# Performance work log

Measured on AMD Instinct MI355X. Metric: run time of the kernel, lower is better.

## Reference

```python
import jax, jax.numpy as jnp
import numpy as np


def l2norm(t, eps=1e-12):
    # matches F.normalize(p=2, dim=-1): divide by norm clamped to eps
    n = jnp.linalg.norm(t, axis=-1, keepdims=True)
    return t / jnp.maximum(n, eps)


def setup_inputs() -> dict:
    key = jax.random.key(0)
    kx, ke = jax.random.split(key)
    B, N, D, C = 8, 1024, 256, 8192
    x = jax.random.normal(kx, (B, N, D), dtype=jnp.float32)
    # codebook initialized l2-normalized, as in __init__ (kmeans_init=False)
    embed = l2norm(jax.random.normal(ke, (1, C, D), dtype=jnp.float32))
    return {"x": x, "embed": embed}


def reference(x, embed):
    # x: [B, N, D]; ndim < 4 -> add codebook dim h=1
    xh = x[None]                                   # [1, B, N, D]
    h, b, n, d = xh.shape
    flat = l2norm(xh.reshape(h, b * n, d))         # [1, B*N, D]
    e = l2norm(embed)                              # [1, C, D]
    # cosine-similarity distances
    dist = jnp.einsum('hnd,hcd->hnc', flat, e)     # [1, B*N, C]
    # sample_codebook_temp == 0 -> plain argmax
    idx = jnp.argmax(dist, axis=-1).reshape(h, b, n)  # [1, B, N]
    # batched_embedding: gather UN-normalized codebook rows
    quantize = jax.vmap(lambda em, ix: em[ix])(embed, idx)  # [1, B, N, D]
    # needs_codebook_dim -> strip leading dim
    return quantize[0], idx[0]
```

## Files before the change

kernel.cpp:

```cpp
#include <hip/hip_runtime.h>
#include <math.h>

#define QROWS 8192
#define DDIM  256
#define CCNT  8192
#define BM    128
#define BN    128
#define BK    64
#define CBLKS (CCNT / BN)

typedef __attribute__((ext_vector_type(4))) float f32x4;
typedef __attribute__((ext_vector_type(8))) short bf16x8;

__device__ __forceinline__ unsigned short f2bf(float f) {
    unsigned u = __float_as_uint(f);
    u += 0x7fffu + ((u >> 16) & 1u);
    return (unsigned short)(u >> 16);
}
__device__ __forceinline__ unsigned u32max(unsigned a, unsigned b) { return a > b ? a : b; }
__device__ __forceinline__ unsigned u32min(unsigned a, unsigned b) { return a < b ? a : b; }

__device__ __forceinline__ unsigned key32(float v, unsigned enc) {
    unsigned u = __float_as_uint(v);
    unsigned s = (unsigned)((int)u >> 31);
    return ((u ^ (s | 0x80000000u)) & 0xFFFFFF80u) | enc;
}

__global__ void k_prep(const float* __restrict__ x, unsigned short* __restrict__ xb,
                       const float* __restrict__ e, unsigned short* __restrict__ eb) {
    const int bid = blockIdx.x;
    if (bid < 1024) {
        const int i = (bid * 256 + threadIdx.x) * 8;
        const float4 f0 = *reinterpret_cast<const float4*>(x + i);
        const float4 f1 = *reinterpret_cast<const float4*>(x + i + 4);
        uint4 o;
        o.x = f2bf(f0.x) | ((unsigned)f2bf(f0.y) << 16);
        o.y = f2bf(f0.z) | ((unsigned)f2bf(f0.w) << 16);
        o.z = f2bf(f1.x) | ((unsigned)f2bf(f1.y) << 16);
        o.w = f2bf(f1.z) | ((unsigned)f2bf(f1.w) << 16);
        *reinterpret_cast<uint4*>(xb + i) = o;
    } else {
        const int row  = (bid - 1024) * 4 + (threadIdx.x >> 6);
        const int lane = threadIdx.x & 63;
        const float4 v = *reinterpret_cast<const float4*>(e + (size_t)row * DDIM + lane * 4);
        float s = v.x * v.x + v.y * v.y + v.z * v.z + v.w * v.w;
        #pragma unroll
        for (int off = 1; off < 64; off <<= 1) s += __shfl_xor(s, off);
        const float inv = 1.0f / fmaxf(sqrtf(s), 1e-12f);
        ushort4 o;
        o.x = f2bf(v.x * inv); o.y = f2bf(v.y * inv);
        o.z = f2bf(v.z * inv); o.w = f2bf(v.w * inv);
        *reinterpret_cast<ushort4*>(eb + (size_t)row * DDIM + lane * 4) = o;
    }
}

#define GLOAD_LDS(g, s) \
    __builtin_amdgcn_global_load_lds((const __attribute__((address_space(1))) void*)(g), \
                                     (__attribute__((address_space(3))) void*)(s), 16, 0, 0)

#define SBAR do { asm volatile("" ::: "memory"); __builtin_amdgcn_s_barrier(); \
                  asm volatile("" ::: "memory"); } while (0)
#define WAIT_LGKM0 do { asm volatile("s_waitcnt lgkmcnt(0)" ::: "memory"); \
                        __builtin_amdgcn_sched_barrier(0); } while (0)
#define WAIT_VM8 do { asm volatile("s_waitcnt vmcnt(8)" ::: "memory"); \
                      __builtin_amdgcn_sched_barrier(0); } while (0)
#define WAIT_VM0 do { asm volatile("s_waitcnt vmcnt(0)" ::: "memory"); \
                      __builtin_amdgcn_sched_barrier(0); } while (0)

__launch_bounds__(256)
__global__ void k_gemm(const unsigned short* __restrict__ xb,
                       const unsigned short* __restrict__ eb,
                       unsigned* pout ) {
    __shared__ __align__(16) char smem[65536];

    const int tid = threadIdx.x;
    const int w = tid >> 6, l = tid & 63;
    const int wr = w >> 1, wc = w & 1;
    const int lg = l >> 4, lr = l & 15;
    const int bx = blockIdx.x, by = blockIdx.y;
    const int n0 = by * BM, c0 = bx * BN;

    const f32x4 zero = {0.f, 0.f, 0.f, 0.f};
    f32x4 acc[4][4];
    #pragma unroll
    for (int i = 0; i < 4; ++i)
        #pragma unroll
        for (int j = 0; j < 4; ++j) acc[i][j] = zero;

    const int srow = tid >> 3;
    const int swzp = (tid & 7) ^ (srow & 7);
    const char* gA = (const char*)xb + (size_t)(n0 + srow) * 512 + swzp * 16;
    const char* gB = (const char*)eb + (size_t)(c0 + srow) * 512 + swzp * 16;
    const int wb = w * 1024;

#define STAGE(Ab, Bb, kb) do {                                          \
    GLOAD_LDS(gA + (kb),         smem + (Ab) + 0 * 4096 + wb);          \
    GLOAD_LDS(gA + (kb) + 16384, smem + (Ab) + 1 * 4096 + wb);          \
    GLOAD_LDS(gA + (kb) + 32768, smem + (Ab) + 2 * 4096 + wb);          \
    GLOAD_LDS(gA + (kb) + 49152, smem + (Ab) + 3 * 4096 + wb);          \
    GLOAD_LDS(gB + (kb),         smem + (Bb) + 0 * 4096 + wb);          \
    GLOAD_LDS(gB + (kb) + 16384, smem + (Bb) + 1 * 4096 + wb);          \
    GLOAD_LDS(gB + (kb) + 32768, smem + (Bb) + 2 * 4096 + wb);          \
    GLOAD_LDS(gB + (kb) + 49152, smem + (Bb) + 3 * 4096 + wb);          \
} while (0)

    const int aoff = (wr * 64 + lr) * 128;
    const int boff = (wc * 64 + lr) * 128;
    const int k0 = ((0 + lg) ^ (lr & 7)) * 16;
    const int k1 = ((4 + lg) ^ (lr & 7)) * 16;

    bf16x8 a[4][2], b[4][2];
#define READS(Ab, Bb) do {                                                           \
    _Pragma("unroll") for (int mi = 0; mi < 4; ++mi) {                               \
        a[mi][0] = *reinterpret_cast<const bf16x8*>(smem + (Ab) + aoff + mi * 2048 + k0); \
        a[mi][1] = *reinterpret_cast<const bf16x8*>(smem + (Ab) + aoff + mi * 2048 + k1); \
    }                                                                                \
    _Pragma("unroll") for (int nj = 0; nj < 4; ++nj) {                               \
        b[nj][0] = *reinterpret_cast<const bf16x8*>(smem + (Bb) + boff + nj * 2048 + k0); \
        b[nj][1] = *reinterpret_cast<const bf16x8*>(smem + (Bb) + boff + nj * 2048 + k1); \
    }                                                                                \
} while (0)

#define MMAS() do {                                                     \
    __builtin_amdgcn_s_setprio(1);                                      \
    _Pragma("unroll") for (int kk = 0; kk < 2; ++kk)                    \
      _Pragma("unroll") for (int mi = 0; mi < 4; ++mi)                  \
        _Pragma("unroll") for (int nj = 0; nj < 4; ++nj)                \
          acc[mi][nj] = __builtin_amdgcn_mfma_f32_16x16x32_bf16(a[mi][kk], b[nj][kk], acc[mi][nj], 0, 0, 0); \
    __builtin_amdgcn_s_setprio(0);                                      \
} while (0)

    STAGE(0, 32768, 0);
    STAGE(16384, 49152, 128);
    WAIT_VM8; SBAR;

    READS(0, 32768);
    WAIT_LGKM0; SBAR;
    STAGE(0, 32768, 256);
    MMAS();
    WAIT_VM8; SBAR;
    READS(16384, 49152);
    WAIT_LGKM0; SBAR;
    STAGE(16384, 49152, 384);
    MMAS();
    WAIT_VM8; SBAR;
    READS(0, 32768);
    WAIT_LGKM0; SBAR;
    MMAS();
    WAIT_VM0; SBAR;
    READS(16384, 49152);
    WAIT_LGKM0;
    MMAS();
    __syncthreads();

    uint2* T = (uint2*)smem;
    const unsigned encbase = (unsigned)(127 - wc * 64 - lr);
    #pragma unroll
    for (int mi = 0; mi < 4; ++mi) {
        #pragma unroll
        for (int r = 0; r < 4; ++r) {
            unsigned q0 = key32(acc[mi][0][r], encbase);
            unsigned q1 = key32(acc[mi][1][r], encbase - 16);
            unsigned q2 = key32(acc[mi][2][r], encbase - 32);
            unsigned q3 = key32(acc[mi][3][r], encbase - 48);
            const unsigned m01 = u32max(q0, q1), n01 = u32min(q0, q1);
            const unsigned m23 = u32max(q2, q3), n23 = u32min(q2, q3);
            const unsigned t1 = u32max(m01, m23);
            const unsigned t2 = u32max(u32min(m01, m23), u32max(n01, n23));
            const int rloc = wr * 64 + mi * 16 + lg * 4 + r;
            uint2 p; p.x = t1; p.y = t2;
            T[rloc * 33 + wc * 16 + lr] = p;
        }
    }
    __syncthreads();

    if (tid < BM) {
        const uint2* rp = T + tid * 33;
        unsigned T1 = 0, T2 = 0;
        #pragma unroll
        for (int i = 0; i < 32; ++i) {
            const uint2 p = rp[i];
            const unsigned n1 = u32max(T1, p.x);
            const unsigned lo = u32min(T1, p.x);
            T2 = u32max(T2, u32max(lo, p.y));
            T1 = n1;
        }
        uint2 o; o.x = T1; o.y = T2;
        *reinterpret_cast<uint2*>(pout + (size_t)(n0 + tid) * 256 + bx * 2) = o;
    }
#undef STAGE
#undef READS
#undef MMAS
}

__device__ __forceinline__ unsigned long long expand_key(unsigned k, int blk) {
    const int col = blk * 128 + 127 - (int)(k & 127u);
    return ((unsigned long long)(k & 0xFFFFFF80u) << 32) | (unsigned)(~col);
}

__global__ void k_fixup(const unsigned* pk,
                        const float* __restrict__ x, const float* __restrict__ e,
                        float* out) {
    const int row = blockIdx.x * 4 + (threadIdx.x >> 6);
    const int t   = threadIdx.x & 63;
    const uint2 kv = reinterpret_cast<const uint2*>(pk + (size_t)row * 256)[t];
    unsigned long long kk0 = expand_key(kv.x, t);
    unsigned long long kk1 = expand_key(kv.y, t);

    int cand[4];
    #pragma unroll
    for (int p = 0; p < 4; ++p) {
        unsigned long long m = kk0 > kk1 ? kk0 : kk1;
        #pragma unroll
        for (int off = 1; off < 64; off <<= 1) {
            const unsigned long long o = __shfl_xor(m, off);
            if (o > m) m = o;
        }
        cand[p] = (int)(~(unsigned)m) & (CCNT - 1);
        if (kk0 == m) kk0 = 0ull;
        if (kk1 == m) kk1 = 0ull;
    }

    const float4 xv = *reinterpret_cast<const float4*>(x + (size_t)row * DDIM + t * 4);
    float best = -INFINITY; int bc = 0x7fffffff;
    #pragma unroll
    for (int p = 0; p < 4; ++p) {
        const int c = cand[p];
        const float4 ev = *reinterpret_cast<const float4*>(e + (size_t)c * DDIM + t * 4);
        float d  = xv.x * ev.x + xv.y * ev.y + xv.z * ev.z + xv.w * ev.w;
        float ss = ev.x * ev.x + ev.y * ev.y + ev.z * ev.z + ev.w * ev.w;
        #pragma unroll
        for (int off = 1; off < 64; off <<= 1) {
            d  += __shfl_xor(d, off);
            ss += __shfl_xor(ss, off);
        }
        const float v = d * (1.0f / fmaxf(sqrtf(ss), 1e-12f));
        if (v > best || (v == best && c < bc)) { best = v; bc = c; }
    }

    if (t == 0) out[(size_t)QROWS * DDIM + row] = (float)bc;
    const float4 q = *reinterpret_cast<const float4*>(e + (size_t)bc * DDIM + t * 4);
    *reinterpret_cast<float4*>(out + (size_t)row * DDIM + t * 4) = q;
}

extern "C" void kernel_launch(void* const* d_in, const int* in_sizes, int n_in,
                              void* d_out, int out_size, void* d_ws, size_t ws_size,
                              hipStream_t stream) {
    const float* x = (const float*)d_in[0];
    const float* e = (const float*)d_in[1];
    float* out = (float*)d_out;
    char* ws = (char*)d_ws;

    unsigned short* xb = (unsigned short*)ws;
    unsigned short* eb = (unsigned short*)(ws + (size_t)4 * 1024 * 1024);

    k_prep<<<3072, 256, 0, stream>>>(x, xb, e, eb);
    dim3 g2(CBLKS, QROWS / BM);
    k_gemm<<<g2, 256, 0, stream>>>(xb, eb, (unsigned*)d_out);
    k_fixup<<<QROWS / 4, 256, 0, stream>>>((const unsigned*)d_out, x, e, out);
}
```

Baseline: 65.54 us.

## Enlarge GEMM tile to 256x256 with 8 waves and looped K pipeline

```diff
diff --git a/kernel.cpp b/kernel.cpp
--- a/kernel.cpp
+++ b/kernel.cpp
@@ -4,9 +4,9 @@
 #define QROWS 8192
 #define DDIM  256
 #define CCNT  8192
-#define BM    128
-#define BN    128
-#define BK    64
+#define BM    256
+#define BN    256
+#define BK    32
 #define CBLKS (CCNT / BN)
 
 typedef __attribute__((ext_vector_type(4))) float f32x4;
@@ -23,7 +23,7 @@
 __device__ __forceinline__ unsigned key32(float v, unsigned enc) {
     unsigned u = __float_as_uint(v);
     unsigned s = (unsigned)((int)u >> 31);
-    return ((u ^ (s | 0x80000000u)) & 0xFFFFFF80u) | enc;
+    return ((u ^ (s | 0x80000000u)) & 0xFFFFFF00u) | enc;
 }
 
 __global__ void k_prep(const float* __restrict__ x, unsigned short* __restrict__ xb,
@@ -62,12 +62,12 @@
                   asm volatile("" ::: "memory"); } while (0)
 #define WAIT_LGKM0 do { asm volatile("s_waitcnt lgkmcnt(0)" ::: "memory"); \
                         __builtin_amdgcn_sched_barrier(0); } while (0)
-#define WAIT_VM8 do { asm volatile("s_waitcnt vmcnt(8)" ::: "memory"); \
+#define WAIT_VM4 do { asm volatile("s_waitcnt vmcnt(4)" ::: "memory"); \
                       __builtin_amdgcn_sched_barrier(0); } while (0)
 #define WAIT_VM0 do { asm volatile("s_waitcnt vmcnt(0)" ::: "memory"); \
                       __builtin_amdgcn_sched_barrier(0); } while (0)
 
-__launch_bounds__(256)
+__launch_bounds__(512, 2)
 __global__ void k_gemm(const unsigned short* __restrict__ xb,
                        const unsigned short* __restrict__ eb,
                        unsigned* pout ) {
@@ -75,127 +75,126 @@
 
     const int tid = threadIdx.x;
     const int w = tid >> 6, l = tid & 63;
-    const int wr = w >> 1, wc = w & 1;
+    const int wr = w >> 2, wc = w & 3;
     const int lg = l >> 4, lr = l & 15;
     const int bx = blockIdx.x, by = blockIdx.y;
     const int n0 = by * BM, c0 = bx * BN;
 
     const f32x4 zero = {0.f, 0.f, 0.f, 0.f};
-    f32x4 acc[4][4];
-    #pragma unroll
-    for (int i = 0; i < 4; ++i)
+    f32x4 acc[8][4];
+    #pragma unroll
+    for (int i = 0; i < 8; ++i)
         #pragma unroll
         for (int j = 0; j < 4; ++j) acc[i][j] = zero;
 
-    const int srow = tid >> 3;
-    const int swzp = (tid & 7) ^ (srow & 7);
-    const char* gA = (const char*)xb + (size_t)(n0 + srow) * 512 + swzp * 16;
-    const char* gB = (const char*)eb + (size_t)(c0 + srow) * 512 + swzp * 16;
+    const int srow = tid >> 2;
+    const int schk = (tid & 3) ^ ((tid >> 3) & 3);
+    const char* gA = (const char*)xb + (size_t)(n0 + srow) * 512 + schk * 16;
+    const char* gB = (const char*)eb + (size_t)(c0 + srow) * 512 + schk * 16;
     const int wb = w * 1024;
 
-#define STAGE(Ab, Bb, kb) do {                                          \
-    GLOAD_LDS(gA + (kb),         smem + (Ab) + 0 * 4096 + wb);          \
-    GLOAD_LDS(gA + (kb) + 16384, smem + (Ab) + 1 * 4096 + wb);          \
-    GLOAD_LDS(gA + (kb) + 32768, smem + (Ab) + 2 * 4096 + wb);          \
-    GLOAD_LDS(gA + (kb) + 49152, smem + (Ab) + 3 * 4096 + wb);          \
-    GLOAD_LDS(gB + (kb),         smem + (Bb) + 0 * 4096 + wb);          \
-    GLOAD_LDS(gB + (kb) + 16384, smem + (Bb) + 1 * 4096 + wb);          \
-    GLOAD_LDS(gB + (kb) + 32768, smem + (Bb) + 2 * 4096 + wb);          \
-    GLOAD_LDS(gB + (kb) + 49152, smem + (Bb) + 3 * 4096 + wb);          \
+#define STAGE(slot, t) do {                                                  \
+    GLOAD_LDS(gA + (t) * 64,         smem + (slot) * 32768 + wb);            \
+    GLOAD_LDS(gA + (t) * 64 + 65536, smem + (slot) * 32768 + 8192 + wb);     \
+    GLOAD_LDS(gB + (t) * 64,         smem + (slot) * 32768 + 16384 + wb);    \
+    GLOAD_LDS(gB + (t) * 64 + 65536, smem + (slot) * 32768 + 24576 + wb);    \
 } while (0)
 
-    const int aoff = (wr * 64 + lr) * 128;
-    const int boff = (wc * 64 + lr) * 128;
-    const int k0 = ((0 + lg) ^ (lr & 7)) * 16;
-    const int k1 = ((4 + lg) ^ (lr & 7)) * 16;
-
-    bf16x8 a[4][2], b[4][2];
-#define READS(Ab, Bb) do {                                                           \
-    _Pragma("unroll") for (int mi = 0; mi < 4; ++mi) {                               \
-        a[mi][0] = *reinterpret_cast<const bf16x8*>(smem + (Ab) + aoff + mi * 2048 + k0); \
-        a[mi][1] = *reinterpret_cast<const bf16x8*>(smem + (Ab) + aoff + mi * 2048 + k1); \
-    }                                                                                \
-    _Pragma("unroll") for (int nj = 0; nj < 4; ++nj) {                               \
-        b[nj][0] = *reinterpret_cast<const bf16x8*>(smem + (Bb) + boff + nj * 2048 + k0); \
-        b[nj][1] = *reinterpret_cast<const bf16x8*>(smem + (Bb) + boff + nj * 2048 + k1); \
-    }                                                                                \
+    const int chkx = (lr >> 1) & 3;
+    const int aoff = (wr * 128 + lr) * 64 + ((lg ^ chkx) * 16);
+    const int boff = 16384 + (wc * 64 + lr) * 64 + ((lg ^ chkx) * 16);
+
+    bf16x8 a[8], b[4];
+#define READS(slot) do {                                                                  \
+    const char* base_ = smem + (slot) * 32768;                                            \
+    _Pragma("unroll") for (int mi = 0; mi < 8; ++mi)                                      \
+        a[mi] = *reinterpret_cast<const bf16x8*>(base_ + aoff + mi * 1024);               \
+    _Pragma("unroll") for (int nj = 0; nj < 4; ++nj)                                      \
+        b[nj] = *reinterpret_cast<const bf16x8*>(base_ + boff + nj * 1024);               \
 } while (0)
 
-#define MMAS() do {                                                     \
-    __builtin_amdgcn_s_setprio(1);                                      \
-    _Pragma("unroll") for (int kk = 0; kk < 2; ++kk)                    \
-      _Pragma("unroll") for (int mi = 0; mi < 4; ++mi)                  \
-        _Pragma("unroll") for (int nj = 0; nj < 4; ++nj)                \
-          acc[mi][nj] = __builtin_amdgcn_mfma_f32_16x16x32_bf16(a[mi][kk], b[nj][kk], acc[mi][nj], 0, 0, 0); \
-    __builtin_amdgcn_s_setprio(0);                                      \
+#define MMAS() do {                                                          \
+    __builtin_amdgcn_s_setprio(1);                                           \
+    _Pragma("unroll") for (int mi = 0; mi < 8; ++mi)                         \
+      _Pragma("unroll") for (int nj = 0; nj < 4; ++nj)                       \
+        acc[mi][nj] = __builtin_amdgcn_mfma_f32_16x16x32_bf16(a[mi], b[nj], acc[mi][nj], 0, 0, 0); \
+    __builtin_amdgcn_s_setprio(0);                                           \
 } while (0)
 
-    STAGE(0, 32768, 0);
-    STAGE(16384, 49152, 128);
-    WAIT_VM8; SBAR;
-
-    READS(0, 32768);
-    WAIT_LGKM0; SBAR;
-    STAGE(0, 32768, 256);
-    MMAS();
-    WAIT_VM8; SBAR;
-    READS(16384, 49152);
-    WAIT_LGKM0; SBAR;
-    STAGE(16384, 49152, 384);
-    MMAS();
-    WAIT_VM8; SBAR;
-    READS(0, 32768);
-    WAIT_LGKM0; SBAR;
-    MMAS();
-    WAIT_VM0; SBAR;
-    READS(16384, 49152);
-    WAIT_LGKM0;
-    MMAS();
+    STAGE(0, 0);
+    STAGE(1, 1);
+    WAIT_VM4; SBAR;
+
+    #pragma unroll
+    for (int t = 0; t < 8; ++t) {
+        const int slot = t & 1;
+        READS(slot);
+        WAIT_LGKM0;
+        SBAR;
+        if (t + 2 < 8) STAGE(slot, t + 2);
+        MMAS();
+        if (t < 7) {
+            if (t < 6) { WAIT_VM4; } else { WAIT_VM0; }
+            SBAR;
+        }
+    }
     __syncthreads();
 
     uint2* T = (uint2*)smem;
-    const unsigned encbase = (unsigned)(127 - wc * 64 - lr);
-    #pragma unroll
-    for (int mi = 0; mi < 4; ++mi) {
-        #pragma unroll
-        for (int r = 0; r < 4; ++r) {
-            unsigned q0 = key32(acc[mi][0][r], encbase);
-            unsigned q1 = key32(acc[mi][1][r], encbase - 16);
-            unsigned q2 = key32(acc[mi][2][r], encbase - 32);
-            unsigned q3 = key32(acc[mi][3][r], encbase - 48);
-            const unsigned m01 = u32max(q0, q1), n01 = u32min(q0, q1);
-            const unsigned m23 = u32max(q2, q3), n23 = u32min(q2, q3);
-            const unsigned t1 = u32max(m01, m23);
-            const unsigned t2 = u32max(u32min(m01, m23), u32max(n01, n23));
-            const int rloc = wr * 64 + mi * 16 + lg * 4 + r;
-            uint2 p; p.x = t1; p.y = t2;
-            T[rloc * 33 + wc * 16 + lr] = p;
-        }
-    }
-    __syncthreads();
-
-    if (tid < BM) {
-        const uint2* rp = T + tid * 33;
-        unsigned T1 = 0, T2 = 0;
-        #pragma unroll
-        for (int i = 0; i < 32; ++i) {
-            const uint2 p = rp[i];
-            const unsigned n1 = u32max(T1, p.x);
-            const unsigned lo = u32min(T1, p.x);
-            T2 = u32max(T2, u32max(lo, p.y));
-            T1 = n1;
-        }
-        uint2 o; o.x = T1; o.y = T2;
-        *reinterpret_cast<uint2*>(pout + (size_t)(n0 + tid) * 256 + bx * 2) = o;
+    const int slotW = wc * 16 + lr;
+    const unsigned encb = 255u - (unsigned)(wc * 64 + lr);
+    #pragma unroll
+    for (int half = 0; half < 2; ++half) {
+        #pragma unroll
+        for (int m = 0; m < 4; ++m) {
+            const int mi = half * 4 + m;
+            #pragma unroll
+            for (int r = 0; r < 4; ++r) {
+                unsigned q0 = key32(acc[mi][0][r], encb);
+                unsigned q1 = key32(acc[mi][1][r], encb - 16);
+                unsigned q2 = key32(acc[mi][2][r], encb - 32);
+                unsigned q3 = key32(acc[mi][3][r], encb - 48);
+                const unsigned m01 = u32max(q0, q1), n01 = u32min(q0, q1);
+                const unsigned m23 = u32max(q2, q3), n23 = u32min(q2, q3);
+                const unsigned t1 = u32max(m01, m23);
+                const unsigned t2 = u32max(u32min(m01, m23), u32max(n01, n23));
+                const int cr = wr * 64 + m * 16 + lg * 4 + r;
+                uint2 p; p.x = t1; p.y = t2;
+                T[cr * 64 + (slotW ^ (cr & 15))] = p;
+            }
+        }
+        __syncthreads();
+        {
+            const int cr = tid >> 2, q = tid & 3;
+            unsigned T1 = 0, T2 = 0;
+            #pragma unroll
+            for (int i = 0; i < 16; ++i) {
+                const uint2 p = T[cr * 64 + ((q * 16 + i) ^ (cr & 15))];
+                const unsigned n1 = u32max(T1, p.x);
+                const unsigned lo = u32min(T1, p.x);
+                T2 = u32max(T2, u32max(lo, p.y));
+                T1 = n1;
+            }
+            #pragma unroll
+            for (int off = 1; off < 4; off <<= 1) {
+                const unsigned o1 = __shfl_xor(T1, off);
+                const unsigned o2 = __shfl_xor(T2, off);
+                const unsigned n1 = u32max(T1, o1);
+                const unsigned lo = u32min(T1, o1);
+                T2 = u32max(u32max(T2, o2), lo);
+                T1 = n1;
+            }
+            if (q == 0) {
+                const int row = n0 + (cr >> 6) * 128 + half * 64 + (cr & 63);
+                uint2 o; o.x = T1; o.y = T2;
+                *reinterpret_cast<uint2*>(pout + (size_t)row * 256 + bx * 2) = o;
+            }
+        }
+        if (half == 0) __syncthreads();
     }
 #undef STAGE
 #undef READS
 #undef MMAS
-}
-
-__device__ __forceinline__ unsigned long long expand_key(unsigned k, int blk) {
-    const int col = blk * 128 + 127 - (int)(k & 127u);
-    return ((unsigned long long)(k & 0xFFFFFF80u) << 32) | (unsigned)(~col);
 }
 
 __global__ void k_fixup(const unsigned* pk,
@@ -203,22 +202,21 @@
                         float* out) {
     const int row = blockIdx.x * 4 + (threadIdx.x >> 6);
     const int t   = threadIdx.x & 63;
-    const uint2 kv = reinterpret_cast<const uint2*>(pk + (size_t)row * 256)[t];
-    unsigned long long kk0 = expand_key(kv.x, t);
-    unsigned long long kk1 = expand_key(kv.y, t);
+    const unsigned k = pk[(size_t)row * 256 + t];
+    const int col0 = (t >> 1) * 256 + 255 - (int)(k & 255u);
+    unsigned long long kk = ((unsigned long long)(k & 0xFFFFFF00u) << 32) | (unsigned)(~col0);
 
     int cand[4];
     #pragma unroll
     for (int p = 0; p < 4; ++p) {
-        unsigned long long m = kk0 > kk1 ? kk0 : kk1;
+        unsigned long long m = kk;
         #pragma unroll
         for (int off = 1; off < 64; off <<= 1) {
             const unsigned long long o = __shfl_xor(m, off);
             if (o > m) m = o;
         }
         cand[p] = (int)(~(unsigned)m) & (CCNT - 1);
-        if (kk0 == m) kk0 = 0ull;
-        if (kk1 == m) kk1 = 0ull;
+        if (kk == m) kk = 0ull;
     }
 
     const float4 xv = *reinterpret_cast<const float4*>(x + (size_t)row * DDIM + t * 4);
@@ -256,6 +254,6 @@
 
     k_prep<<<3072, 256, 0, stream>>>(x, xb, e, eb);
     dim3 g2(CBLKS, QROWS / BM);
-    k_gemm<<<g2, 256, 0, stream>>>(xb, eb, (unsigned*)d_out);
+    k_gemm<<<g2, 512, 0, stream>>>(xb, eb, (unsigned*)d_out);
     k_fixup<<<QROWS / 4, 256, 0, stream>>>((const unsigned*)d_out, x, e, out);
 }
```

After: 68.32 us. 4.2% more time.
